# Kernel tuning notes

Measured on AMD Instinct MI355X. Metric: run time of the kernel, lower is better.

The kernel has to match this reference:

```python
import jax, jax.numpy as jnp
import numpy as np

COMMITMENT_COST = 0.25


def setup_inputs() -> dict:
    key = jax.random.key(0)
    k1, k2 = jax.random.split(key)
    B, C, L, H, W = 4, 64, 16, 32, 32
    K = 1024
    inputs = jax.random.normal(k1, (B, C, L, H, W), dtype=jnp.float32)
    # matches torch init: uniform_(-1/K, 1/K)
    codebook = jax.random.uniform(k2, (K, C), dtype=jnp.float32,
                                  minval=-1.0 / K, maxval=1.0 / K)
    return {"inputs": inputs, "codebook": codebook}


def reference(inputs, codebook):
    B, C, L, H, W = inputs.shape
    # [B,C,L,H,W] -> [N, D] with D == embedding_dim == C
    x = jnp.transpose(inputs, (0, 2, 3, 4, 1)).reshape(-1, C).astype(jnp.float32)
    cb = codebook.astype(jnp.float32)
    # squared euclidean distances (argmin identical to p=2 cdist argmin)
    d2 = (jnp.sum(x * x, axis=1, keepdims=True)
          - 2.0 * (x @ cb.T)
          + jnp.sum(cb * cb, axis=1))  # [N, K]
    encoding_indices = jnp.argmin(d2, axis=1)  # [N]
    # one-hot @ codebook == direct gather
    quantized = cb[encoding_indices].astype(inputs.dtype)  # [N, D]
    quantized = jnp.transpose(quantized.reshape(B, L, H, W, C), (0, 4, 1, 2, 3))
    e_latent_loss = jnp.mean((jax.lax.stop_gradient(quantized) - inputs) ** 2)
    q_latent_loss = jnp.mean((quantized - jax.lax.stop_gradient(inputs)) ** 2)
    loss = q_latent_loss + COMMITMENT_COST * e_latent_loss
    # straight-through estimator
    quantized_st = inputs + jax.lax.stop_gradient(quantized - inputs)
    return quantized_st, loss, encoding_indices[:, None]
```

## Files before the change

### kernel.cpp

```cpp
#include <hip/hip_runtime.h>

constexpr int Cc   = 64;
constexpr int Kc   = 1024;
constexpr int Dc   = 64;
constexpr int LHWc = 16 * 32 * 32;
constexpr int Nc   = 4 * LHWc;
constexpr int QSIZE    = 4 * Cc * LHWc;
constexpr int OFF_LOSS = QSIZE;
constexpr int OFF_IDX  = QSIZE + 1;

constexpr int BLK_ROWS = 128;
constexpr int NW       = 8;

typedef __attribute__((ext_vector_type(8))) short short8;
typedef __attribute__((ext_vector_type(4))) float f32x4;

static __device__ __forceinline__ unsigned short f2bf(float f) {
    unsigned u = __float_as_uint(f);
    u += 0x7FFFu + ((u >> 16) & 1u);
    return (unsigned short)(u >> 16);
}
static __device__ __forceinline__ float bf2f(unsigned short h) {
    return __uint_as_float(((unsigned)h) << 16);
}

__global__ __launch_bounds__(256) void vq_prep(
    const float* __restrict__ cb, float* __restrict__ out,
    unsigned short* __restrict__ cbh, unsigned short* __restrict__ cbl,
    float* __restrict__ c2, float* __restrict__ c2n)
{
    const int t  = threadIdx.x;
    const int k0 = blockIdx.x * 64;
    if (blockIdx.x == 0 && t == 0) out[OFF_LOSS] = 0.0f;

    const int d  = t & 63;
#pragma unroll
    for (int r = 0; r < 16; ++r) {
        const int k = k0 + r * 4 + (t >> 6);
        const float v = cb[(size_t)k * Dc + d];
        unsigned short h = f2bf(v);
        cbh[(size_t)k * Dc + d] = h;
        cbl[(size_t)k * Dc + d] = f2bf(v - bf2f(h));
    }
    if (t < 64) {
        const int k = k0 + t;
        const float* c = cb + (size_t)k * Dc;
        float s = 0.f;
#pragma unroll
        for (int dd = 0; dd < Dc; ++dd) s = __builtin_fmaf(c[dd], c[dd], s);
        c2[k]  = s;
        c2n[k] = -0.5f * (s + 0.25f);
    }
}

__global__ __launch_bounds__(512, 2) void vq_main(
    const float* __restrict__ in, const float* __restrict__ codebook,
    const unsigned short* __restrict__ cbh,
    const unsigned short* __restrict__ cbl,
    const float* __restrict__ c2g, const float* __restrict__ c2ng,
    float* __restrict__ out)
{
    __shared__ short8   xfh[1024];
    __shared__ short8   xfl[1024];
    __shared__ float    c2ns[Kc];
    __shared__ float    xpart[BLK_ROWS][8];
    __shared__ float    xs2[BLK_ROWS];
    __shared__ float    cV1[NW][BLK_ROWS];
    __shared__ float    cV2[NW][BLK_ROWS];
    __shared__ unsigned cK [NW][BLK_ROWS];
    __shared__ unsigned kpack[BLK_ROWS];

    const int tid  = threadIdx.x;
    const int lane = tid & 63;
    const int w    = __builtin_amdgcn_readfirstlane(tid >> 6);
    const int col  = lane & 15;
    const int g    = lane >> 4;

    const int bq = blockIdx.x >> 7;
    const int p0 = (blockIdx.x & 127) * BLK_ROWS;
    const size_t inBase = (size_t)bq * (Cc * LHWc) + p0;

    c2ns[tid]       = c2ng[tid];
    c2ns[tid + 512] = c2ng[tid + 512];

#pragma unroll
    for (int jj = 0; jj < 2; ++jj) {
        const int c  = tid + jj * 512;
        const int t  = c >> 7;
        const int kt = (c >> 6) & 1;
        const int gi = (c >> 4) & 3;
        const int cl = c & 15;
        const int row = t * 16 + cl;
        const float* xp = in + inBase + (size_t)(kt * 32 + gi * 8) * LHWc + row;
        float v[8];
#pragma unroll
        for (int j = 0; j < 8; ++j) v[j] = xp[(size_t)j * LHWc];
        float p = 0.f;
#pragma unroll
        for (int j = 0; j < 8; ++j) p = __builtin_fmaf(v[j], v[j], p);
        short8 h8, l8;
#pragma unroll
        for (int j = 0; j < 8; ++j) {
            unsigned short hv = f2bf(v[j]);
            h8[j] = (short)hv;
            l8[j] = (short)f2bf(v[j] - bf2f(hv));
        }
        xfh[c] = h8; xfl[c] = l8;
        xpart[row][kt * 4 + gi] = p;
    }

    short8 Ah[8][2], Al[8][2];
#pragma unroll
    for (int ct = 0; ct < 8; ++ct) {
        const size_t cb0 = (size_t)(w * 128 + ct * 16 + col) * Dc + g * 8;
#pragma unroll
        for (int kt = 0; kt < 2; ++kt) {
            Ah[ct][kt] = *(const short8*)(cbh + cb0 + kt * 32);
            Al[ct][kt] = *(const short8*)(cbl + cb0 + kt * 32);
        }
    }
    __syncthreads();

    if (tid < BLK_ROWS) {
        const float* q = xpart[tid];
        xs2[tid] = ((q[0] + q[1]) + (q[2] + q[3])) + ((q[4] + q[5]) + (q[6] + q[7]));
    }

#pragma unroll 1
    for (int t = 0; t < 8; ++t) {
        const short8 xh0 = xfh[t * 128 + lane];
        const short8 xh1 = xfh[t * 128 + 64 + lane];
        const short8 xl0 = xfl[t * 128 + lane];
        const short8 xl1 = xfl[t * 128 + 64 + lane];

        float bV = -3.4e38f, sV = -3.4e38f;
        int   bK = 0, sK = 0;

#pragma unroll
        for (int ct = 0; ct < 8; ++ct) {
            f32x4 acc = *(const f32x4*)&c2ns[w * 128 + ct * 16 + g * 4];
            acc = __builtin_amdgcn_mfma_f32_16x16x32_bf16(Ah[ct][0], xh0, acc, 0, 0, 0);
            acc = __builtin_amdgcn_mfma_f32_16x16x32_bf16(Ah[ct][1], xh1, acc, 0, 0, 0);
            acc = __builtin_amdgcn_mfma_f32_16x16x32_bf16(Ah[ct][0], xl0, acc, 0, 0, 0);
            acc = __builtin_amdgcn_mfma_f32_16x16x32_bf16(Ah[ct][1], xl1, acc, 0, 0, 0);
            acc = __builtin_amdgcn_mfma_f32_16x16x32_bf16(Al[ct][0], xh0, acc, 0, 0, 0);
            acc = __builtin_amdgcn_mfma_f32_16x16x32_bf16(Al[ct][1], xh1, acc, 0, 0, 0);
#pragma unroll
            for (int r = 0; r < 4; ++r) {
                const float a = acc[r];
                const int   k = w * 128 + ct * 16 + g * 4 + r;
                bool  c1 = a > bV;
                float nb  = c1 ? a : bV;
                int   nbk = c1 ? k : bK;
                float mn  = c1 ? bV : a;
                int   mnk = c1 ? bK : k;
                bool  c2_ = mn > sV;
                sV = c2_ ? mn : sV;
                sK = c2_ ? mnk : sK;
                bV = nb; bK = nbk;
            }
        }

#pragma unroll
        for (int m = 16; m <= 32; m <<= 1) {
            float ob  = __shfl_xor(bV, m, 64);
            int   obk = __shfl_xor(bK, m, 64);
            float os  = __shfl_xor(sV, m, 64);
            int   osk = __shfl_xor(sK, m, 64);
            bool  c1 = ob > bV;
            float nb  = c1 ? ob : bV;
            int   nbk = c1 ? obk : bK;
            float mn  = c1 ? bV : ob;
            int   mnk = c1 ? bK : obk;
            bool  c3 = os > sV;
            float ms  = c3 ? os : sV;
            int   msk = c3 ? osk : sK;
            bool  c4 = mn > ms;
            sV = c4 ? mn : ms;
            sK = c4 ? mnk : msk;
            bV = nb; bK = nbk;
        }
        if (g == 0) {
            const int row = t * 16 + col;
            cV1[w][row] = bV;
            cV2[w][row] = sV;
            cK [w][row] = (unsigned)bK | ((unsigned)sK << 16);
        }
    }
    __syncthreads();

    if (tid < 2 * BLK_ROWS) {
        const int row = tid >> 1;
        const int h   = tid & 1;
        float b = -3.4e38f, s = -3.4e38f;
        int   bk = 0, sk = 0;
#pragma unroll
        for (int wv = 0; wv < 4; ++wv) {
            const int wj = h * 4 + wv;
            const unsigned ks = cK[wj][row];
            const float v1 = cV1[wj][row];
            const float v2 = cV2[wj][row];
            const int  k1 = (int)(ks & 0xFFFFu);
            const int  k2 = (int)(ks >> 16);
            {
                bool c1 = v1 > b;
                float mn = c1 ? b : v1;  int mnk = c1 ? bk : k1;
                b  = c1 ? v1 : b;        bk  = c1 ? k1 : bk;
                bool c2_ = mn > s;  s = c2_ ? mn : s;  sk = c2_ ? mnk : sk;
            }
            {
                bool c1 = v2 > b;
                float mn = c1 ? b : v2;  int mnk = c1 ? bk : k2;
                b  = c1 ? v2 : b;        bk  = c1 ? k2 : bk;
                bool c2_ = mn > s;  s = c2_ ? mn : s;  sk = c2_ ? mnk : sk;
            }
        }
        float ob  = __shfl_xor(b, 1, 64);
        int   obk = __shfl_xor(bk, 1, 64);
        float os  = __shfl_xor(s, 1, 64);
        int   osk = __shfl_xor(sk, 1, 64);
        if (h == 0) {
            bool  c1 = ob > b;
            float nb  = c1 ? ob : b;
            int   nbk = c1 ? obk : bk;
            float mn  = c1 ? b : ob;
            int   mnk = c1 ? bk : obk;
            bool  c3 = os > s;
            float ms  = c3 ? os : s;
            int   msk = c3 ? osk : sk;
            bool  c4 = mn > ms;
            int   fsk = c4 ? mnk : msk;
            kpack[row] = (unsigned)nbk | ((unsigned)fsk << 16);
        }
    }
    __syncthreads();

    if (tid < 2 * BLK_ROWS) {
        const int row = tid >> 1;
        const int ci  = tid & 1;
        const unsigned pr = kpack[row];
        const int k = ci ? (int)(pr >> 16) : (int)(pr & 0xFFFFu);
        const float* cbr = codebook + (size_t)k * Dc;
        const float* xr  = in + inBase + row;
        float a0 = 0.f, a1 = 0.f, a2 = 0.f, a3 = 0.f;
#pragma unroll
        for (int d = 0; d < 64; d += 4) {
            a0 = __builtin_fmaf(xr[(size_t)(d + 0) * LHWc], cbr[d + 0], a0);
            a1 = __builtin_fmaf(xr[(size_t)(d + 1) * LHWc], cbr[d + 1], a1);
            a2 = __builtin_fmaf(xr[(size_t)(d + 2) * LHWc], cbr[d + 2], a2);
            a3 = __builtin_fmaf(xr[(size_t)(d + 3) * LHWc], cbr[d + 3], a3);
        }
        float a  = (a0 + a1) + (a2 + a3);
        float d2 = __builtin_fmaf(-2.f, a, xs2[row]) + c2g[k];
        unsigned long long pk =
            ((unsigned long long)__float_as_uint(d2) << 32) | (unsigned)k;
        unsigned long long o = __shfl_xor(pk, 1, 64);
        pk = o < pk ? o : pk;
        if (ci == 0) {
            const int kwin = (int)(pk & 0x3FFu);
            kpack[row] = (unsigned)kwin;
            out[OFF_IDX + (size_t)blockIdx.x * BLK_ROWS + row] = (float)kwin;
        }
    }
    __syncthreads();

    {
        const int row = tid & 127;
        const int cp  = tid >> 7;
        const int kw  = (int)kpack[row];
        const float* cbw = codebook + (size_t)kw * Dc + cp * 16;
        const float* xr  = in + inBase + row;
        float* qout = out + inBase + row;
        float ls = 0.f;
#pragma unroll
        for (int j = 0; j < 16; ++j) {
            const int c = cp * 16 + j;
            float qv = cbw[j];
            qout[(size_t)c * LHWc] = qv;
            float e = qv - xr[(size_t)c * LHWc];
            ls = __builtin_fmaf(e, e, ls);
        }
#pragma unroll
        for (int off = 32; off > 0; off >>= 1) ls += __shfl_down(ls, off, 64);
        if (lane == 0) atomicAdd(&out[OFF_LOSS], ls * (1.25f / (float)QSIZE));
    }
}

extern "C" void kernel_launch(void* const* d_in, const int* in_sizes, int n_in,
                              void* d_out, int out_size, void* d_ws, size_t ws_size,
                              hipStream_t stream) {
    const float* in = (const float*)d_in[0];
    const float* cb = (const float*)d_in[1];
    float* out = (float*)d_out;
    (void)in_sizes; (void)n_in; (void)out_size; (void)ws_size;

    unsigned short* cbh = (unsigned short*)d_ws;
    unsigned short* cbl = cbh + (size_t)Kc * Dc;
    float*          c2  = (float*)(cbl + (size_t)Kc * Dc);
    float*          c2n = c2 + Kc;

    vq_prep<<<dim3(16), dim3(256), 0, stream>>>(cb, out, cbh, cbl, c2, c2n);
    vq_main<<<dim3(Nc / BLK_ROWS), dim3(512), 0, stream>>>(in, cb, cbh, cbl, c2, c2n, out);
}
```

Before: 159.8 us.

## Double rows per block, interleave two MFMA chains, exact-rescore all per-wave candidates

Doubles BLK_ROWS to 256 so each workgroup reuses its register-resident codebook fragments across twice as many rows, halving the grid. Each wave now runs two independent MFMA accumulation chains in an interleaved order to hide MFMA latency, and keeps the c2 seeds in registers instead of LDS. The LDS-based two-stage top-2 merge is dropped: each thread loads its full 64-float row and exactly rescores all 8 top-2 candidates from its 4 waves in fp32, then merges with its partner lane. This trades more global reads and more fp32 FMA per row, plus higher register pressure and half as many blocks, for fewer barriers and more MFMA work per codebook load.

```diff
diff --git a/kernel.cpp b/kernel.cpp
--- a/kernel.cpp
+++ b/kernel.cpp
@@ -9,7 +9,7 @@
 constexpr int OFF_LOSS = QSIZE;
 constexpr int OFF_IDX  = QSIZE + 1;
 
-constexpr int BLK_ROWS = 128;
+constexpr int BLK_ROWS = 256;
 constexpr int NW       = 8;
 
 typedef __attribute__((ext_vector_type(8))) short short8;
@@ -60,15 +60,10 @@
     const float* __restrict__ c2g, const float* __restrict__ c2ng,
     float* __restrict__ out)
 {
-    __shared__ short8   xfh[1024];
-    __shared__ short8   xfl[1024];
-    __shared__ float    c2ns[Kc];
-    __shared__ float    xpart[BLK_ROWS][8];
-    __shared__ float    xs2[BLK_ROWS];
-    __shared__ float    cV1[NW][BLK_ROWS];
-    __shared__ float    cV2[NW][BLK_ROWS];
-    __shared__ unsigned cK [NW][BLK_ROWS];
-    __shared__ unsigned kpack[BLK_ROWS];
+    __shared__ short8   xfh[2048];
+    __shared__ short8   xfl[2048];
+    __shared__ unsigned cK[NW][BLK_ROWS];
+    __shared__ unsigned kwin[BLK_ROWS];
 
     const int tid  = threadIdx.x;
     const int lane = tid & 63;
@@ -76,16 +71,26 @@
     const int col  = lane & 15;
     const int g    = lane >> 4;
 
-    const int bq = blockIdx.x >> 7;
-    const int p0 = (blockIdx.x & 127) * BLK_ROWS;
+    const int bq = blockIdx.x >> 6;
+    const int p0 = (blockIdx.x & 63) * BLK_ROWS;
     const size_t inBase = (size_t)bq * (Cc * LHWc) + p0;
 
-    c2ns[tid]       = c2ng[tid];
-    c2ns[tid + 512] = c2ng[tid + 512];
-
-#pragma unroll
-    for (int jj = 0; jj < 2; ++jj) {
-        const int c  = tid + jj * 512;
+    short8 Ah[8][2], Al[8][2];
+    f32x4  seed[8];
+#pragma unroll
+    for (int ct = 0; ct < 8; ++ct) {
+        const size_t cb0 = (size_t)(w * 128 + ct * 16 + col) * Dc + g * 8;
+#pragma unroll
+        for (int kt = 0; kt < 2; ++kt) {
+            Ah[ct][kt] = *(const short8*)(cbh + cb0 + kt * 32);
+            Al[ct][kt] = *(const short8*)(cbl + cb0 + kt * 32);
+        }
+        seed[ct] = *(const f32x4*)&c2ng[w * 128 + ct * 16 + g * 4];
+    }
+
+#pragma unroll
+    for (int j = 0; j < 4; ++j) {
+        const int c  = tid + j * 512;
         const int t  = c >> 7;
         const int kt = (c >> 6) & 1;
         const int gi = (c >> 4) & 3;
@@ -94,187 +99,172 @@
         const float* xp = in + inBase + (size_t)(kt * 32 + gi * 8) * LHWc + row;
         float v[8];
 #pragma unroll
-        for (int j = 0; j < 8; ++j) v[j] = xp[(size_t)j * LHWc];
-        float p = 0.f;
-#pragma unroll
-        for (int j = 0; j < 8; ++j) p = __builtin_fmaf(v[j], v[j], p);
+        for (int e = 0; e < 8; ++e) v[e] = xp[(size_t)e * LHWc];
         short8 h8, l8;
 #pragma unroll
-        for (int j = 0; j < 8; ++j) {
-            unsigned short hv = f2bf(v[j]);
-            h8[j] = (short)hv;
-            l8[j] = (short)f2bf(v[j] - bf2f(hv));
+        for (int e = 0; e < 8; ++e) {
+            unsigned short hv = f2bf(v[e]);
+            h8[e] = (short)hv;
+            l8[e] = (short)f2bf(v[e] - bf2f(hv));
         }
         xfh[c] = h8; xfl[c] = l8;
-        xpart[row][kt * 4 + gi] = p;
-    }
-
-    short8 Ah[8][2], Al[8][2];
-#pragma unroll
-    for (int ct = 0; ct < 8; ++ct) {
-        const size_t cb0 = (size_t)(w * 128 + ct * 16 + col) * Dc + g * 8;
-#pragma unroll
-        for (int kt = 0; kt < 2; ++kt) {
-            Ah[ct][kt] = *(const short8*)(cbh + cb0 + kt * 32);
-            Al[ct][kt] = *(const short8*)(cbl + cb0 + kt * 32);
-        }
     }
     __syncthreads();
 
-    if (tid < BLK_ROWS) {
-        const float* q = xpart[tid];
-        xs2[tid] = ((q[0] + q[1]) + (q[2] + q[3])) + ((q[4] + q[5]) + (q[6] + q[7]));
-    }
-
 #pragma unroll 1
-    for (int t = 0; t < 8; ++t) {
-        const short8 xh0 = xfh[t * 128 + lane];
-        const short8 xh1 = xfh[t * 128 + 64 + lane];
-        const short8 xl0 = xfl[t * 128 + lane];
-        const short8 xl1 = xfl[t * 128 + 64 + lane];
-
-        float bV = -3.4e38f, sV = -3.4e38f;
-        int   bK = 0, sK = 0;
+    for (int tp = 0; tp < 8; ++tp) {
+        const int b0 = tp * 256;
+        const int b1 = tp * 256 + 128;
+        const short8 xh0a = xfh[b0 + lane],      xh1a = xfh[b0 + 64 + lane];
+        const short8 xl0a = xfl[b0 + lane],      xl1a = xfl[b0 + 64 + lane];
+        const short8 xh0b = xfh[b1 + lane],      xh1b = xfh[b1 + 64 + lane];
+        const short8 xl0b = xfl[b1 + lane],      xl1b = xfl[b1 + 64 + lane];
+
+        float bV0 = -3.4e38f, sV0 = -3.4e38f, bV1 = -3.4e38f, sV1 = -3.4e38f;
+        int   bK0 = 0, sK0 = 0, bK1 = 0, sK1 = 0;
 
 #pragma unroll
         for (int ct = 0; ct < 8; ++ct) {
-            f32x4 acc = *(const f32x4*)&c2ns[w * 128 + ct * 16 + g * 4];
-            acc = __builtin_amdgcn_mfma_f32_16x16x32_bf16(Ah[ct][0], xh0, acc, 0, 0, 0);
-            acc = __builtin_amdgcn_mfma_f32_16x16x32_bf16(Ah[ct][1], xh1, acc, 0, 0, 0);
-            acc = __builtin_amdgcn_mfma_f32_16x16x32_bf16(Ah[ct][0], xl0, acc, 0, 0, 0);
-            acc = __builtin_amdgcn_mfma_f32_16x16x32_bf16(Ah[ct][1], xl1, acc, 0, 0, 0);
-            acc = __builtin_amdgcn_mfma_f32_16x16x32_bf16(Al[ct][0], xh0, acc, 0, 0, 0);
-            acc = __builtin_amdgcn_mfma_f32_16x16x32_bf16(Al[ct][1], xh1, acc, 0, 0, 0);
+            f32x4 a0 = seed[ct];
+            f32x4 a1 = seed[ct];
+            a0 = __builtin_amdgcn_mfma_f32_16x16x32_bf16(Ah[ct][0], xh0a, a0, 0, 0, 0);
+            a1 = __builtin_amdgcn_mfma_f32_16x16x32_bf16(Ah[ct][0], xh0b, a1, 0, 0, 0);
+            a0 = __builtin_amdgcn_mfma_f32_16x16x32_bf16(Ah[ct][1], xh1a, a0, 0, 0, 0);
+            a1 = __builtin_amdgcn_mfma_f32_16x16x32_bf16(Ah[ct][1], xh1b, a1, 0, 0, 0);
+            a0 = __builtin_amdgcn_mfma_f32_16x16x32_bf16(Ah[ct][0], xl0a, a0, 0, 0, 0);
+            a1 = __builtin_amdgcn_mfma_f32_16x16x32_bf16(Ah[ct][0], xl0b, a1, 0, 0, 0);
+            a0 = __builtin_amdgcn_mfma_f32_16x16x32_bf16(Ah[ct][1], xl1a, a0, 0, 0, 0);
+            a1 = __builtin_amdgcn_mfma_f32_16x16x32_bf16(Ah[ct][1], xl1b, a1, 0, 0, 0);
+            a0 = __builtin_amdgcn_mfma_f32_16x16x32_bf16(Al[ct][0], xh0a, a0, 0, 0, 0);
+            a1 = __builtin_amdgcn_mfma_f32_16x16x32_bf16(Al[ct][0], xh0b, a1, 0, 0, 0);
+            a0 = __builtin_amdgcn_mfma_f32_16x16x32_bf16(Al[ct][1], xh1a, a0, 0, 0, 0);
+            a1 = __builtin_amdgcn_mfma_f32_16x16x32_bf16(Al[ct][1], xh1b, a1, 0, 0, 0);
 #pragma unroll
             for (int r = 0; r < 4; ++r) {
-                const float a = acc[r];
-                const int   k = w * 128 + ct * 16 + g * 4 + r;
-                bool  c1 = a > bV;
-                float nb  = c1 ? a : bV;
-                int   nbk = c1 ? k : bK;
-                float mn  = c1 ? bV : a;
-                int   mnk = c1 ? bK : k;
-                bool  c2_ = mn > sV;
-                sV = c2_ ? mn : sV;
-                sK = c2_ ? mnk : sK;
-                bV = nb; bK = nbk;
+                const int k = w * 128 + ct * 16 + g * 4 + r;
+                {
+                    const float a = a0[r];
+                    const float ob = bV0; const int obk = bK0;
+                    const bool c1 = a > ob;
+                    const bool c2_ = a > sV0;
+                    bV0 = c1 ? a : ob;
+                    sV0 = fmaxf(fminf(a, ob), sV0);
+                    bK0 = c1 ? k : obk;
+                    sK0 = c2_ ? (c1 ? obk : k) : sK0;
+                }
+                {
+                    const float a = a1[r];
+                    const float ob = bV1; const int obk = bK1;
+                    const bool c1 = a > ob;
+                    const bool c2_ = a > sV1;
+                    bV1 = c1 ? a : ob;
+                    sV1 = fmaxf(fminf(a, ob), sV1);
+                    bK1 = c1 ? k : obk;
+                    sK1 = c2_ ? (c1 ? obk : k) : sK1;
+                }
             }
         }
 
 #pragma unroll
         for (int m = 16; m <= 32; m <<= 1) {
-            float ob  = __shfl_xor(bV, m, 64);
-            int   obk = __shfl_xor(bK, m, 64);
-            float os  = __shfl_xor(sV, m, 64);
-            int   osk = __shfl_xor(sK, m, 64);
-            bool  c1 = ob > bV;
-            float nb  = c1 ? ob : bV;
-            int   nbk = c1 ? obk : bK;
-            float mn  = c1 ? bV : ob;
-            int   mnk = c1 ? bK : obk;
-            bool  c3 = os > sV;
-            float ms  = c3 ? os : sV;
-            int   msk = c3 ? osk : sK;
-            bool  c4 = mn > ms;
-            sV = c4 ? mn : ms;
-            sK = c4 ? mnk : msk;
-            bV = nb; bK = nbk;
+            {
+                float ob  = __shfl_xor(bV0, m, 64);
+                int   obk = __shfl_xor(bK0, m, 64);
+                float os  = __shfl_xor(sV0, m, 64);
+                int   osk = __shfl_xor(sK0, m, 64);
+                bool  c1 = ob > bV0;
+                float nb  = c1 ? ob : bV0;
+                int   nbk = c1 ? obk : bK0;
+                float mn  = c1 ? bV0 : ob;
+                int   mnk = c1 ? bK0 : obk;
+                bool  c3 = os > sV0;
+                float ms  = c3 ? os : sV0;
+                int   msk = c3 ? osk : sK0;
+                bool  c4 = mn > ms;
+                sV0 = c4 ? mn : ms;  sK0 = c4 ? mnk : msk;
+                bV0 = nb;            bK0 = nbk;
+            }
+            {
+                float ob  = __shfl_xor(bV1, m, 64);
+                int   obk = __shfl_xor(bK1, m, 64);
+                float os  = __shfl_xor(sV1, m, 64);
+                int   osk = __shfl_xor(sK1, m, 64);
+                bool  c1 = ob > bV1;
+                float nb  = c1 ? ob : bV1;
+                int   nbk = c1 ? obk : bK1;
+                float mn  = c1 ? bV1 : ob;
+                int   mnk = c1 ? bK1 : obk;
+                bool  c3 = os > sV1;
+                float ms  = c3 ? os : sV1;
+                int   msk = c3 ? osk : sK1;
+                bool  c4 = mn > ms;
+                sV1 = c4 ? mn : ms;  sK1 = c4 ? mnk : msk;
+                bV1 = nb;            bK1 = nbk;
+            }
         }
         if (g == 0) {
-            const int row = t * 16 + col;
-            cV1[w][row] = bV;
-            cV2[w][row] = sV;
-            cK [w][row] = (unsigned)bK | ((unsigned)sK << 16);
+            cK[w][tp * 32 + col]      = (unsigned)bK0 | ((unsigned)sK0 << 16);
+            cK[w][tp * 32 + 16 + col] = (unsigned)bK1 | ((unsigned)sK1 << 16);
         }
     }
     __syncthreads();
 
-    if (tid < 2 * BLK_ROWS) {
+    {
         const int row = tid >> 1;
         const int h   = tid & 1;
-        float b = -3.4e38f, s = -3.4e38f;
-        int   bk = 0, sk = 0;
+        float x[64];
+        const float* xr = in + inBase + row;
+#pragma unroll
+        for (int d = 0; d < 64; ++d) x[d] = xr[(size_t)d * LHWc];
+
+        float x2 = 0.f;
+#pragma unroll
+        for (int d = 0; d < 64; ++d) x2 = __builtin_fmaf(x[d], x[d], x2);
+
+        unsigned long long best = ~0ull;
 #pragma unroll
         for (int wv = 0; wv < 4; ++wv) {
-            const int wj = h * 4 + wv;
-            const unsigned ks = cK[wj][row];
-            const float v1 = cV1[wj][row];
-            const float v2 = cV2[wj][row];
-            const int  k1 = (int)(ks & 0xFFFFu);
-            const int  k2 = (int)(ks >> 16);
-            {
-                bool c1 = v1 > b;
-                float mn = c1 ? b : v1;  int mnk = c1 ? bk : k1;
-                b  = c1 ? v1 : b;        bk  = c1 ? k1 : bk;
-                bool c2_ = mn > s;  s = c2_ ? mn : s;  sk = c2_ ? mnk : sk;
-            }
-            {
-                bool c1 = v2 > b;
-                float mn = c1 ? b : v2;  int mnk = c1 ? bk : k2;
-                b  = c1 ? v2 : b;        bk  = c1 ? k2 : bk;
-                bool c2_ = mn > s;  s = c2_ ? mn : s;  sk = c2_ ? mnk : sk;
-            }
-        }
-        float ob  = __shfl_xor(b, 1, 64);
-        int   obk = __shfl_xor(bk, 1, 64);
-        float os  = __shfl_xor(s, 1, 64);
-        int   osk = __shfl_xor(sk, 1, 64);
+            const unsigned ks = cK[h * 4 + wv][row];
+#pragma unroll
+            for (int ci = 0; ci < 2; ++ci) {
+                const int k = ci ? (int)(ks >> 16) : (int)(ks & 0xFFFFu);
+                const float* cbr = codebook + (size_t)k * Dc;
+                float a0 = 0.f, a1 = 0.f, a2 = 0.f, a3 = 0.f;
+#pragma unroll
+                for (int d = 0; d < 64; d += 4) {
+                    a0 = __builtin_fmaf(x[d + 0], cbr[d + 0], a0);
+                    a1 = __builtin_fmaf(x[d + 1], cbr[d + 1], a1);
+                    a2 = __builtin_fmaf(x[d + 2], cbr[d + 2], a2);
+                    a3 = __builtin_fmaf(x[d + 3], cbr[d + 3], a3);
+                }
+                const float a  = (a0 + a1) + (a2 + a3);
+                const float d2 = __builtin_fmaf(-2.f, a, x2) + c2g[k];
+                unsigned long long pk =
+                    ((unsigned long long)__float_as_uint(d2) << 32) | (unsigned)k;
+                best = pk < best ? pk : best;
+            }
+        }
+        unsigned long long o = __shfl_xor(best, 1, 64);
+        best = o < best ? o : best;
         if (h == 0) {
-            bool  c1 = ob > b;
-            float nb  = c1 ? ob : b;
-            int   nbk = c1 ? obk : bk;
-            float mn  = c1 ? b : ob;
-            int   mnk = c1 ? bk : obk;
-            bool  c3 = os > s;
-            float ms  = c3 ? os : s;
-            int   msk = c3 ? osk : sk;
-            bool  c4 = mn > ms;
-            int   fsk = c4 ? mnk : msk;
-            kpack[row] = (unsigned)nbk | ((unsigned)fsk << 16);
+            const int kwinv = (int)(best & 0x3FFu);
+            kwin[row] = (unsigned)kwinv;
+            out[OFF_IDX + (size_t)blockIdx.x * BLK_ROWS + row] = (float)kwinv;
         }
     }
     __syncthreads();
 
-    if (tid < 2 * BLK_ROWS) {
-        const int row = tid >> 1;
-        const int ci  = tid & 1;
-        const unsigned pr = kpack[row];
-        const int k = ci ? (int)(pr >> 16) : (int)(pr & 0xFFFFu);
-        const float* cbr = codebook + (size_t)k * Dc;
-        const float* xr  = in + inBase + row;
-        float a0 = 0.f, a1 = 0.f, a2 = 0.f, a3 = 0.f;
-#pragma unroll
-        for (int d = 0; d < 64; d += 4) {
-            a0 = __builtin_fmaf(xr[(size_t)(d + 0) * LHWc], cbr[d + 0], a0);
-            a1 = __builtin_fmaf(xr[(size_t)(d + 1) * LHWc], cbr[d + 1], a1);
-            a2 = __builtin_fmaf(xr[(size_t)(d + 2) * LHWc], cbr[d + 2], a2);
-            a3 = __builtin_fmaf(xr[(size_t)(d + 3) * LHWc], cbr[d + 3], a3);
-        }
-        float a  = (a0 + a1) + (a2 + a3);
-        float d2 = __builtin_fmaf(-2.f, a, xs2[row]) + c2g[k];
-        unsigned long long pk =
-            ((unsigned long long)__float_as_uint(d2) << 32) | (unsigned)k;
-        unsigned long long o = __shfl_xor(pk, 1, 64);
-        pk = o < pk ? o : pk;
-        if (ci == 0) {
-            const int kwin = (int)(pk & 0x3FFu);
-            kpack[row] = (unsigned)kwin;
-            out[OFF_IDX + (size_t)blockIdx.x * BLK_ROWS + row] = (float)kwin;
-        }
-    }
-    __syncthreads();
-
     {
-        const int row = tid & 127;
-        const int cp  = tid >> 7;
-        const int kw  = (int)kpack[row];
-        const float* cbw = codebook + (size_t)kw * Dc + cp * 16;
+        const int row = tid & 255;
+        const int cp  = tid >> 8;
+        const int kw  = (int)kwin[row];
+        const float* cbw = codebook + (size_t)kw * Dc + cp * 32;
         const float* xr  = in + inBase + row;
         float* qout = out + inBase + row;
         float ls = 0.f;
 #pragma unroll
-        for (int j = 0; j < 16; ++j) {
-            const int c = cp * 16 + j;
+        for (int j = 0; j < 32; ++j) {
+            const int c = cp * 32 + j;
             float qv = cbw[j];
             qout[(size_t)c * LHWc] = qv;
             float e = qv - xr[(size_t)c * LHWc];
```

After: 163.2 us. 1.02x slower.
